# Kernel optimization log

Measured on AMD Instinct MI355X. Metric: run time of the kernel, lower is better.

## Reference

```python
import jax, jax.numpy as jnp
import numpy as np

NUM_RBF = 16
TOP_K = 30
MAXREL = 32  # max_relative_feature
M_CTX = 16   # ligand context atoms per residue

PT_GROUP = jnp.array([0,1,18,1,2,13,14,15,16,17,18,1,2,13,14,15,16,17,18,1,2,3,4,5,6,7,8,9,10,11,12,13,14,15,16,17,18,1,2,3,4,5,6,7,8,9,10,11,12,13,14,15,16,17,18,1,2,3,3,3,3,3,3,3,3,3,3,3,3,3,3,3,4,5,6,7,8,9,10,11,12,13,14,15,16,17,18,1,2,3,3,3,3,3,3,3,3,3,3,3,3,3,3,3,4,5,6,7,8,9,10,11,12,13,14,15,16,17,18], dtype=jnp.int32)
PT_PERIOD = jnp.array([0,1,1,2,2,2,2,2,2,2,2,3,3,3,3,3,3,3,3,4,4,4,4,4,4,4,4,4,4,4,4,4,4,4,4,4,4,5,5,5,5,5,5,5,5,5,5,5,5,5,5,5,5,5,5,6,6,6,6,6,6,6,6,6,6,6,6,6,6,6,6,6,6,6,6,6,6,6,6,6,6,6,6,6,6,6,6,7,7,7,7,7,7,7,7,7,7,7,7,7,7,7,7,7,7,7,7,7,7,7,7,7,7,7,7,7,7,7,7], dtype=jnp.int32)

# pair order after the Ca-Ca term: (N,N),(C,C),(O,O),(Cb,Cb),(Ca,N),(Ca,C),(Ca,O),(Ca,Cb),
# (N,C),(N,O),(N,Cb),(Cb,C),(Cb,O),(O,C),(N,Ca),(C,Ca),(O,Ca),(Cb,Ca),(C,N),(O,N),(Cb,N),(C,Cb),(O,Cb),(C,O)
# atom index in A5 stack: N=0, Ca=1, C=2, O=3, Cb=4
AI = np.array([0,2,3,4,1,1,1,1,0,0,0,4,4,3,0,2,3,4,2,3,4,2,3,2])
BI = np.array([0,2,3,4,0,2,3,4,2,3,4,2,3,2,1,1,1,1,0,0,0,4,4,3])


def _rbf(D):
    mu = jnp.linspace(2.0, 22.0, NUM_RBF)
    sigma = (22.0 - 2.0) / NUM_RBF
    return jnp.exp(-(((D[..., None] - mu) / sigma) ** 2))


def _angle_features(A, Bc, Cc, Y):
    v1 = A - Bc
    v2 = Cc - Bc
    e1 = v1 / jnp.linalg.norm(v1, axis=-1, keepdims=True)
    dot = jnp.einsum('bli,bli->bl', e1, v2)[..., None]
    u2 = v2 - e1 * dot
    e2 = u2 / jnp.linalg.norm(u2, axis=-1, keepdims=True)
    e3 = jnp.cross(e1, e2, axis=-1)
    R = jnp.concatenate((e1[..., None], e2[..., None], e3[..., None]), axis=-1)  # [B,L,3,3]
    lv = jnp.einsum('blqp,blyq->blyp', R, Y - Bc[:, :, None, :])
    rxy = jnp.sqrt(lv[..., 0] ** 2 + lv[..., 1] ** 2 + 1e-8)
    f1 = lv[..., 0] / rxy
    f2 = lv[..., 1] / rxy
    rxyz = jnp.linalg.norm(lv, axis=-1) + 1e-8
    f3 = rxy / rxyz
    f4 = lv[..., 2] / rxyz
    return jnp.stack([f1, f2, f3, f4], axis=-1)  # [B,L,M,4]


def setup_inputs() -> dict:
    key = jax.random.key(0)
    ks = jax.random.split(key, 16)
    B, L, M = 2, 2048, M_CTX
    X = jax.random.normal(ks[0], (B, L, 4, 3), jnp.float32) * 10.0
    Y = jax.random.normal(ks[1], (B, L, M, 3), jnp.float32) * 10.0
    mask = jnp.ones((B, L), jnp.float32)
    Y_m = jnp.ones((B, L, M), jnp.float32)
    R_idx = jnp.arange(B * L, dtype=jnp.int32).reshape(B, L)
    chain_labels = jax.random.randint(ks[2], (B, L), 0, 2, jnp.int32)
    Y_t = jax.random.randint(ks[3], (B, L, M), 1, 119, jnp.int32)
    def lin(k, fi, fo):
        return jax.random.normal(k, (fi, fo), jnp.float32) / np.sqrt(fi)
    params = dict(
        Wp=lin(ks[4], 2 * MAXREL + 2, 16), bp=jnp.zeros((16,), jnp.float32),
        We=lin(ks[5], 16 + 25 * NUM_RBF, 128), be=jnp.zeros((128,), jnp.float32),
        Wn=lin(ks[6], 5 * NUM_RBF + 64 + 4, 128), bn=jnp.zeros((128,), jnp.float32),
        Wt=lin(ks[7], 147, 64), bt=jnp.zeros((64,), jnp.float32),
        Wyn=lin(ks[8], 147, 128), byn=jnp.zeros((128,), jnp.float32),
        Wye=lin(ks[9], NUM_RBF, 128), bye=jnp.zeros((128,), jnp.float32),
    )
    return dict(X=X, Y=Y, mask=mask, Y_m=Y_m, R_idx=R_idx, chain_labels=chain_labels, Y_t=Y_t, **params)


def reference(X, Y, mask, Y_m, R_idx, chain_labels, Y_t,
              Wp, bp, We, be, Wn, bn, Wt, bt, Wyn, byn, Wye, bye):
    B, L = X.shape[0], X.shape[1]
    N, Ca, C, O = X[:, :, 0], X[:, :, 1], X[:, :, 2], X[:, :, 3]
    b_ = Ca - N
    c_ = C - Ca
    a_ = jnp.cross(b_, c_, axis=-1)
    Cb = -0.58273431 * a_ + 0.56802827 * b_ - 0.54067466 * c_ + Ca

    # masked pairwise distances + kNN (smallest-k)
    m2 = mask[:, None, :] * mask[:, :, None]
    dX = Ca[:, None, :, :] - Ca[:, :, None, :]
    D = m2 * jnp.sqrt(jnp.sum(dX * dX, -1) + 1e-6)
    Dadj = D + (1.0 - m2) * jnp.max(D, -1, keepdims=True)
    k = min(TOP_K, L)
    negD, E_idx = jax.lax.top_k(-Dadj, k)
    D_neighbors = -negD  # [B,L,K]

    # gather all 5 atom coords of neighbors once, then all 24 cross-atom RBFs
    A5 = jnp.stack([N, Ca, C, O, Cb], axis=2)  # [B,L,5,3]
    nb = A5[jnp.arange(B)[:, None, None], E_idx]  # [B,L,K,5,3]
    dvec = A5[:, :, None, AI, :] - nb[:, :, :, BI, :]  # [B,L,K,24,3]
    Dp = jnp.sqrt(jnp.sum(dvec * dvec, -1) + 1e-6)
    RBF_all = jnp.concatenate([_rbf(D_neighbors),
                               _rbf(Dp).reshape(B, L, k, 24 * NUM_RBF)], axis=-1)  # [B,L,K,400]

    # positional encodings
    offset = jnp.take_along_axis(R_idx[:, :, None] - R_idx[:, None, :], E_idx, axis=2)
    Ech = jnp.take_along_axis((chain_labels[:, :, None] == chain_labels[:, None, :]).astype(jnp.int32), E_idx, axis=2)
    d = jnp.clip(offset + MAXREL, 0, 2 * MAXREL)
    d = d * Ech + (1 - Ech) * (2 * MAXREL + 1)
    Epos = jax.nn.one_hot(d, 2 * MAXREL + 2, dtype=jnp.float32) @ Wp + bp
    E = jnp.concatenate([Epos, RBF_all], axis=-1) @ We + be  # [B,L,K,128]

    # ligand atom featurization
    g = PT_GROUP[Y_t]
    p = PT_PERIOD[Y_t]
    Yt1 = jnp.concatenate([jax.nn.one_hot(Y_t, 120, dtype=jnp.float32),
                           jax.nn.one_hot(g, 19, dtype=jnp.float32),
                           jax.nn.one_hot(p, 8, dtype=jnp.float32)], axis=-1)  # [B,L,M,147]
    Yt_lin = Yt1 @ Wt + bt  # [B,L,M,64]
    dAY = A5[:, :, :, None, :] - Y[:, :, None, :, :]  # [B,L,5,M,3]
    D_AY = jnp.sqrt(jnp.sum(dAY * dAY, -1) + 1e-6)
    RBF_AY = jnp.transpose(_rbf(D_AY), (0, 1, 3, 2, 4)).reshape(B, L, Y.shape[2], 5 * NUM_RBF)
    f_ang = _angle_features(N, Ca, C, Y)  # [B,L,M,4]
    V = jnp.concatenate([RBF_AY, Yt_lin, f_ang], axis=-1) @ Wn + bn  # [B,L,M,128]

    dYY = Y[:, :, :, None, :] - Y[:, :, None, :, :]
    Y_edges = _rbf(jnp.sqrt(jnp.sum(dYY * dYY, -1) + 1e-6)) @ Wye + bye  # [B,L,M,M,128]
    Y_nodes = Yt1 @ Wyn + byn  # [B,L,M,128]
    return V, E, E_idx, Y_nodes, Y_edges, Y_m
```

## Files before the change

kernel.cpp:

```cpp
#include <hip/hip_runtime.h>
#include <float.h>

typedef unsigned int   u32;
typedef unsigned short ushort_t;
typedef __attribute__((ext_vector_type(8))) short  bf16x8;
typedef __attribute__((ext_vector_type(4))) float  f32x4;
typedef __attribute__((ext_vector_type(8))) unsigned short ushort8;

#define NB 2
#define NL 2048
#define NM 16
#define NK 30

#define OV  0ull
#define OE  8388608ull
#define OEI 24117248ull
#define OYN 24240128ull
#define OYE 32628736ull
#define OYM 166846464ull

__constant__ int PT_GROUP_c[119] = {0,1,18,1,2,13,14,15,16,17,18,1,2,13,14,15,16,17,18,1,2,3,4,5,6,7,8,9,10,11,12,13,14,15,16,17,18,1,2,3,4,5,6,7,8,9,10,11,12,13,14,15,16,17,18,1,2,3,3,3,3,3,3,3,3,3,3,3,3,3,3,3,4,5,6,7,8,9,10,11,12,13,14,15,16,17,18,1,2,3,3,3,3,3,3,3,3,3,3,3,3,3,3,3,4,5,6,7,8,9,10,11,12,13,14,15,16,17,18};
__constant__ int PT_PERIOD_c[119] = {0,1,1,2,2,2,2,2,2,2,2,3,3,3,3,3,3,3,3,4,4,4,4,4,4,4,4,4,4,4,4,4,4,4,4,4,4,5,5,5,5,5,5,5,5,5,5,5,5,5,5,5,5,5,5,6,6,6,6,6,6,6,6,6,6,6,6,6,6,6,6,6,6,6,6,6,6,6,6,6,6,6,6,6,6,6,6,7,7,7,7,7,7,7,7,7,7,7,7,7,7,7,7,7,7,7,7,7,7,7,7,7,7,7,7,7,7,7,7};
__constant__ int AI_c[24] = {0,2,3,4,1,1,1,1,0,0,0,4,4,3,0,2,3,4,2,3,4,2,3,2};
__constant__ int BI_c[24] = {0,2,3,4,0,2,3,4,2,3,4,2,3,2,1,1,1,1,0,0,0,4,4,3};

__device__ __forceinline__ float cl24(float v) {
  return fminf(fmaxf(v, -24.f), 24.f);
}

__device__ __forceinline__ ushort_t f2bf(float f) {
  u32 u = __float_as_uint(f);
  return (ushort_t)((u + 0x7fffu + ((u >> 16) & 1u)) >> 16);
}

__device__ __forceinline__ float rbff(float d, int r) {
  float mu = 2.0f + (20.0f / 15.0f) * (float)r;
  float t = (d - mu) * 0.8f;
  return __expf(-t * t);
}

__global__ __launch_bounds__(256) void k_init(const float* __restrict__ We,
        const float* __restrict__ Wn, const float* __restrict__ X,
        ushort_t* __restrict__ WeT, ushort_t* __restrict__ WnT,
        float* __restrict__ A5, float* __restrict__ Ca4,
        float* __restrict__ Fr,
        const int* __restrict__ Y_t, const float* __restrict__ Wyn,
        const float* __restrict__ byn, const float* __restrict__ Y_m,
        float* __restrict__ out) {
  int blk = blockIdx.x;
  int tid = threadIdx.x;
  if (blk < 128) {
    int n = blk;
    int ntile = n >> 4, ln = n & 15;
    for (int k = tid; k < 416; k += 256) {
      int c = k >> 5, r = k & 31, hk = r >> 3, e = r & 7;
      WeT[(size_t)((ntile * 13 + c) * 512) + (hk * 16 + ln) * 8 + e] =
          f2bf(We[(size_t)k * 128 + n]);
    }
    return;
  }
  if (blk < 256) {
    int n = blk - 128;
    int ntile = n >> 4, ln = n & 15;
    if (tid < 160) {
      int c = tid >> 5, r = tid & 31, hk = r >> 3, e = r & 7;
      WnT[(size_t)((ntile * 5 + c) * 512) + (hk * 16 + ln) * 8 + e] =
          (tid < 148) ? f2bf(Wn[(size_t)tid * 128 + n]) : (ushort_t)0;
    }
    return;
  }
  if (blk < 272) {
    int id = (blk - 256) * 256 + tid;
    if (id >= NB * NL) return;
    const float* x = X + (size_t)id * 12;
    float Nx=x[0],Ny=x[1],Nz=x[2], Cax=x[3],Cay=x[4],Caz=x[5];
    float Cx=x[6],Cy=x[7],Cz=x[8], Ox=x[9],Oy=x[10],Oz=x[11];
    float bx=Cax-Nx, by=Cay-Ny, bz=Caz-Nz;
    float cx=Cx-Cax, cy=Cy-Cay, cz=Cz-Caz;
    float ax=by*cz-bz*cy, ay=bz*cx-bx*cz, az=bx*cy-by*cx;
    float Cbx = -0.58273431f*ax + 0.56802827f*bx - 0.54067466f*cx + Cax;
    float Cby = -0.58273431f*ay + 0.56802827f*by - 0.54067466f*cy + Cay;
    float Cbz = -0.58273431f*az + 0.56802827f*bz - 0.54067466f*cz + Caz;
    float* A = A5 + (size_t)id * 15;
    A[0]=Nx;A[1]=Ny;A[2]=Nz; A[3]=Cax;A[4]=Cay;A[5]=Caz;
    A[6]=Cx;A[7]=Cy;A[8]=Cz; A[9]=Ox;A[10]=Oy;A[11]=Oz;
    A[12]=Cbx;A[13]=Cby;A[14]=Cbz;
    Ca4[id*4+0]=Cax; Ca4[id*4+1]=Cay; Ca4[id*4+2]=Caz; Ca4[id*4+3]=0.f;
    float v1x=Nx-Cax, v1y=Ny-Cay, v1z=Nz-Caz;
    float v2x=Cx-Cax, v2y=Cy-Cay, v2z=Cz-Caz;
    float n1 = sqrtf(v1x*v1x+v1y*v1y+v1z*v1z);
    float e1x=v1x/n1, e1y=v1y/n1, e1z=v1z/n1;
    float dot = e1x*v2x+e1y*v2y+e1z*v2z;
    float u2x=v2x-e1x*dot, u2y=v2y-e1y*dot, u2z=v2z-e1z*dot;
    float n2 = sqrtf(u2x*u2x+u2y*u2y+u2z*u2z);
    float e2x=u2x/n2, e2y=u2y/n2, e2z=u2z/n2;
    float e3x=e1y*e2z-e1z*e2y, e3y=e1z*e2x-e1x*e2z, e3z=e1x*e2y-e1y*e2x;
    float* F = Fr + (size_t)id * 9;
    F[0]=e1x;F[1]=e1y;F[2]=e1z; F[3]=e2x;F[4]=e2y;F[5]=e2z; F[6]=e3x;F[7]=e3y;F[8]=e3z;
    return;
  }
  {
    int bl = blk - 272;
    if (tid < NM)
      out[OYM + (size_t)bl * NM + tid] = Y_m[(size_t)bl * NM + tid];
    int m = tid >> 4, n0 = (tid & 15) * 8;
    int yt = Y_t[(size_t)bl * NM + m];
    int g = PT_GROUP_c[yt], p = PT_PERIOD_c[yt];
    const float* w0 = Wyn + yt * 128 + n0;
    const float* w1 = Wyn + (120 + g) * 128 + n0;
    const float* w2 = Wyn + (139 + p) * 128 + n0;
    float4 r0 = *(const float4*)&w0[0], r1 = *(const float4*)&w0[4];
    float4 s0 = *(const float4*)&w1[0], s1 = *(const float4*)&w1[4];
    float4 t0 = *(const float4*)&w2[0], t1 = *(const float4*)&w2[4];
    float4 b0 = *(const float4*)&byn[n0], b1 = *(const float4*)&byn[n0 + 4];
    float4 o0, o1;
    o0.x = cl24(r0.x + s0.x + t0.x + b0.x);
    o0.y = cl24(r0.y + s0.y + t0.y + b0.y);
    o0.z = cl24(r0.z + s0.z + t0.z + b0.z);
    o0.w = cl24(r0.w + s0.w + t0.w + b0.w);
    o1.x = cl24(r1.x + s1.x + t1.x + b1.x);
    o1.y = cl24(r1.y + s1.y + t1.y + b1.y);
    o1.z = cl24(r1.z + s1.z + t1.z + b1.z);
    o1.w = cl24(r1.w + s1.w + t1.w + b1.w);
    size_t ob = OYN + ((size_t)bl * NM + m) * 128 + n0;
    *(float4*)&out[ob]     = o0;
    *(float4*)&out[ob + 4] = o1;
  }
}

__global__ __launch_bounds__(256) void k_topk(const float* __restrict__ Ca4,
                                              const float* __restrict__ mask,
                                              float* __restrict__ Dn,
                                              int* __restrict__ Eidx,
                                              float* __restrict__ out) {
  __shared__ float dist[NL];
  __shared__ float rv[4];
  __shared__ float cand_v[128];
  __shared__ int   cand_i[128];
  int row = blockIdx.x;
  int b = row >> 11;
  int tid = threadIdx.x;
  const float4* cab = (const float4*)Ca4 + ((size_t)b << 11);
  float4 ci = ((const float4*)Ca4)[row];
  float mi = mask[row];
  float lmax = 0.f;
  for (int j = tid; j < NL; j += 256) {
    float4 cj = cab[j];
    float dx = __fsub_rn(ci.x, cj.x);
    float dy = __fsub_rn(ci.y, cj.y);
    float dz = __fsub_rn(ci.z, cj.z);
    float s  = __fadd_rn(__fadd_rn(__fadd_rn(__fmul_rn(dx,dx), __fmul_rn(dy,dy)),
                                   __fmul_rn(dz,dz)), 1e-6f);
    float D  = __fmul_rn(__fmul_rn(mask[(b << 11) + j], mi), __fsqrt_rn(s));
    dist[j] = D;
    lmax = fmaxf(lmax, D);
  }
  #pragma unroll
  for (int s = 32; s > 0; s >>= 1) lmax = fmaxf(lmax, __shfl_xor(lmax, s));
  if ((tid & 63) == 0) rv[tid >> 6] = lmax;
  __syncthreads();
  float rowmax = fmaxf(fmaxf(rv[0], rv[1]), fmaxf(rv[2], rv[3]));
  for (int j = tid; j < NL; j += 256) {
    float mj = mask[(b << 11) + j];
    dist[j] = __fadd_rn(dist[j], __fmul_rn(__fsub_rn(1.f, __fmul_rn(mi, mj)), rowmax));
  }
  __syncthreads();
  int w = tid >> 6, l = tid & 63;
  int base = w * 512 + l;
  float v[8];
  #pragma unroll
  for (int k = 0; k < 8; k++) v[k] = dist[base + k * 64];
  if (tid < 8) { cand_v[120 + tid] = FLT_MAX; cand_i[120 + tid] = NL; }
  for (int it = 0; it < NK; it++) {
    float bv = FLT_MAX; int bj = NL;
    #pragma unroll
    for (int k = 0; k < 8; k++) {
      int jj = base + k * 64;
      if (v[k] < bv) { bv = v[k]; bj = jj; }
    }
    #pragma unroll
    for (int s = 32; s > 0; s >>= 1) {
      float ov = __shfl_xor(bv, s);
      int   oj = __shfl_xor(bj, s);
      if (ov < bv || (ov == bv && oj < bj)) { bv = ov; bj = oj; }
    }
    int ow = bj & 511;
    int ko = ow >> 6;
    bool mine = (ow & 63) == l;
    #pragma unroll
    for (int k = 0; k < 8; k++)
      if (mine && k == ko) v[k] = FLT_MAX;
    if (l == 0) { cand_v[w * NK + it] = bv; cand_i[w * NK + it] = bj; }
  }
  __syncthreads();
  if (tid < 64) {
    float v1 = cand_v[tid], v2 = cand_v[64 + tid];
    int   i1 = cand_i[tid], i2 = cand_i[64 + tid];
    for (int it = 0; it < NK; it++) {
      float bv; int bj, sl;
      if (v1 < v2 || (v1 == v2 && i1 < i2)) { bv = v1; bj = i1; sl = tid; }
      else                                  { bv = v2; bj = i2; sl = 64 + tid; }
      #pragma unroll
      for (int s = 32; s > 0; s >>= 1) {
        float ov = __shfl_xor(bv, s);
        int   oj = __shfl_xor(bj, s);
        int   os = __shfl_xor(sl, s);
        if (ov < bv || (ov == bv && oj < bj)) { bv = ov; bj = oj; sl = os; }
      }
      if (sl == tid)           v1 = FLT_MAX;
      else if (sl == 64 + tid) v2 = FLT_MAX;
      if (tid == 0) {
        Dn[(size_t)row * NK + it]   = bv;
        Eidx[(size_t)row * NK + it] = bj;
        out[OEI + (size_t)row * NK + it] = (float)bj;
      }
    }
  }
}

__global__ __launch_bounds__(256) void k_edge(const float* __restrict__ A5,
        const float* __restrict__ Dn, const int* __restrict__ Eidx,
        const int* __restrict__ R_idx, const int* __restrict__ cl,
        const float* __restrict__ Wp, const float* __restrict__ bp,
        const ushort_t* __restrict__ WeT, const float* __restrict__ be,
        float* __restrict__ out) {
  __shared__ __align__(16) ushort_t feat[32][424];
  int tid = threadIdx.x;
  int e0 = blockIdx.x * 32;
  {
    int el = tid >> 3;
    int te = tid & 7;
    int e  = e0 + el;
    int bi = e / NK;
    int b  = bi >> 11;
    int j  = Eidx[e];
    j = j < 0 ? 0 : (j > NL - 1 ? NL - 1 : j);
    int jrow = (b << 11) + j;
    const float* Ac = A5 + (size_t)bi * 15;
    const float* An = A5 + (size_t)jrow * 15;
    int off = R_idx[bi] - R_idx[jrow];
    int d;
    if (cl[bi] == cl[jrow]) { d = off + 32; d = d < 0 ? 0 : (d > 64 ? 64 : d); }
    else d = 65;
    feat[el][2*te]   = f2bf(Wp[d * 16 + 2*te]   + bp[2*te]);
    feat[el][2*te+1] = f2bf(Wp[d * 16 + 2*te+1] + bp[2*te+1]);
    float dn = Dn[e];
    feat[el][16 + 2*te]   = f2bf(rbff(dn, 2*te));
    feat[el][16 + 2*te+1] = f2bf(rbff(dn, 2*te+1));
    #pragma unroll
    for (int pp = 0; pp < 3; pp++) {
      int p = te + pp * 8;
      int ai = AI_c[p] * 3, bj2 = BI_c[p] * 3;
      float dx = Ac[ai]   - An[bj2];
      float dy = Ac[ai+1] - An[bj2+1];
      float dz = Ac[ai+2] - An[bj2+2];
      float dp = sqrtf(dx*dx + dy*dy + dz*dz + 1e-6f);
      int fb = 32 + p * 16;
      #pragma unroll
      for (int r = 0; r < 16; r++) feat[el][fb + r] = f2bf(rbff(dp, r));
    }
  }
  __syncthreads();
  int l  = tid & 63;
  int wid = tid >> 6;
  int wm = wid >> 1, wn = wid & 1;
  f32x4 acc0 = {0.f,0.f,0.f,0.f}, acc1 = {0.f,0.f,0.f,0.f};
  f32x4 acc2 = {0.f,0.f,0.f,0.f}, acc3 = {0.f,0.f,0.f,0.f};
  const ushort_t* Wb = WeT + l * 8;
  #pragma unroll 2
  for (int c = 0; c < 13; c++) {
    bf16x8 a  = *(const bf16x8*)&feat[wm*16 + (l & 15)][c*32 + (l >> 4)*8];
    bf16x8 b0 = *(const bf16x8*)(Wb + ((wn*4 + 0)*13 + c)*512);
    bf16x8 b1 = *(const bf16x8*)(Wb + ((wn*4 + 1)*13 + c)*512);
    bf16x8 b2 = *(const bf16x8*)(Wb + ((wn*4 + 2)*13 + c)*512);
    bf16x8 b3 = *(const bf16x8*)(Wb + ((wn*4 + 3)*13 + c)*512);
    acc0 = __builtin_amdgcn_mfma_f32_16x16x32_bf16(a, b0, acc0, 0, 0, 0);
    acc1 = __builtin_amdgcn_mfma_f32_16x16x32_bf16(a, b1, acc1, 0, 0, 0);
    acc2 = __builtin_amdgcn_mfma_f32_16x16x32_bf16(a, b2, acc2, 0, 0, 0);
    acc3 = __builtin_amdgcn_mfma_f32_16x16x32_bf16(a, b3, acc3, 0, 0, 0);
  }
  #pragma unroll
  for (int t = 0; t < 4; t++) {
    f32x4 av = (t==0) ? acc0 : (t==1) ? acc1 : (t==2) ? acc2 : acc3;
    int n = wn*64 + t*16 + (l & 15);
    float bb = be[n];
    #pragma unroll
    for (int jj = 0; jj < 4; jj++) {
      int ee = e0 + wm*16 + (l >> 4)*4 + jj;
      out[OE + (size_t)ee * 128 + n] = cl24(av[jj] + bb);
    }
  }
}

__global__ __launch_bounds__(256) void k_v(const float* __restrict__ A5,
        const float* __restrict__ Fr, const float* __restrict__ Y,
        const int* __restrict__ Y_t,
        const ushort_t* __restrict__ WnT, const float* __restrict__ bn,
        const float* __restrict__ Wt, const float* __restrict__ bt,
        float* __restrict__ out) {
  __shared__ __align__(16) ushort_t feat[16][168];
  __shared__ float dAY[16][8];
  int tid = threadIdx.x;
  int bl = blockIdx.x;
  if (tid < 80) {
    int m = tid / 5, a = tid % 5;
    float dx = A5[(size_t)bl*15 + a*3 + 0] - Y[(size_t)bl*48 + m*3 + 0];
    float dy = A5[(size_t)bl*15 + a*3 + 1] - Y[(size_t)bl*48 + m*3 + 1];
    float dz = A5[(size_t)bl*15 + a*3 + 2] - Y[(size_t)bl*48 + m*3 + 2];
    dAY[m][a] = sqrtf(dx*dx + dy*dy + dz*dz + 1e-6f);
  }
  __syncthreads();
  {
    int m = tid >> 4, q = tid & 15;
    #pragma unroll
    for (int a = 0; a < 5; a++) feat[m][a * 16 + q] = f2bf(rbff(dAY[m][a], q));
    int yt = Y_t[(size_t)bl * NM + m];
    int g = PT_GROUP_c[yt], p = PT_PERIOD_c[yt];
    {
      float4 wa = *(const float4*)&Wt[yt*64 + q*4];
      float4 wb = *(const float4*)&Wt[(120+g)*64 + q*4];
      float4 wc = *(const float4*)&Wt[(139+p)*64 + q*4];
      float4 bb = *(const float4*)&bt[q*4];
      feat[m][80 + q*4 + 0] = f2bf(wa.x + wb.x + wc.x + bb.x);
      feat[m][80 + q*4 + 1] = f2bf(wa.y + wb.y + wc.y + bb.y);
      feat[m][80 + q*4 + 2] = f2bf(wa.z + wb.z + wc.z + bb.z);
      feat[m][80 + q*4 + 3] = f2bf(wa.w + wb.w + wc.w + bb.w);
    }
    if (q == 0) {
      const float* fr = Fr + (size_t)bl * 9;
      float cax = A5[(size_t)bl*15+3], cay = A5[(size_t)bl*15+4], caz = A5[(size_t)bl*15+5];
      float yx = Y[(size_t)bl*48 + m*3+0] - cax;
      float yy = Y[(size_t)bl*48 + m*3+1] - cay;
      float yz = Y[(size_t)bl*48 + m*3+2] - caz;
      float l0 = fr[0]*yx + fr[1]*yy + fr[2]*yz;
      float l1 = fr[3]*yx + fr[4]*yy + fr[5]*yz;
      float l2 = fr[6]*yx + fr[7]*yy + fr[8]*yz;
      float rxy  = sqrtf(l0*l0 + l1*l1 + 1e-8f);
      float rxyz = sqrtf(l0*l0 + l1*l1 + l2*l2) + 1e-8f;
      feat[m][144] = f2bf(l0 / rxy);
      feat[m][145] = f2bf(l1 / rxy);
      feat[m][146] = f2bf(rxy / rxyz);
      feat[m][147] = f2bf(l2 / rxyz);
    }
    if (q < 12) feat[m][148 + q] = 0;
  }
  __syncthreads();
  int l = tid & 63;
  int wid = tid >> 6;
  int n0 = wid * 32;
  f32x4 acc0 = {0.f,0.f,0.f,0.f}, acc1 = {0.f,0.f,0.f,0.f};
  const ushort_t* Wb = WnT + l * 8;
  #pragma unroll
  for (int c = 0; c < 5; c++) {
    bf16x8 a  = *(const bf16x8*)&feat[l & 15][c*32 + (l >> 4)*8];
    bf16x8 b0 = *(const bf16x8*)(Wb + ((2*wid + 0)*5 + c)*512);
    bf16x8 b1 = *(const bf16x8*)(Wb + ((2*wid + 1)*5 + c)*512);
    acc0 = __builtin_amdgcn_mfma_f32_16x16x32_bf16(a, b0, acc0, 0, 0, 0);
    acc1 = __builtin_amdgcn_mfma_f32_16x16x32_bf16(a, b1, acc1, 0, 0, 0);
  }
  #pragma unroll
  for (int t = 0; t < 2; t++) {
    f32x4 av = (t==0) ? acc0 : acc1;
    int n = n0 + t*16 + (l & 15);
    float bb = bn[n];
    #pragma unroll
    for (int jj = 0; jj < 4; jj++) {
      int m = (l >> 4)*4 + jj;
      out[OV + ((size_t)bl * NM + m) * 128 + n] = cl24(av[jj] + bb);
    }
  }
}

__global__ __launch_bounds__(256) void k_yedge(const float* __restrict__ Y,
        const float* __restrict__ Wye, const float* __restrict__ bye,
        float* __restrict__ out) {
  __shared__ float rbf_s[128][20];
  __shared__ float wye_s[16][128];
  __shared__ float bye_s[128];
  int tid = threadIdx.x;
  int bl   = blockIdx.x >> 1;
  int half = blockIdx.x & 1;
  for (int x = tid; x < 2048; x += 256) wye_s[x >> 7][x & 127] = Wye[x];
  if (tid < 128) bye_s[tid] = bye[tid];
  {
    int lp = tid >> 1, rh = (tid & 1) * 8;
    int p = half * 128 + lp;
    int m = p >> 4, m2 = p & 15;
    const float* ya = Y + (size_t)bl * 48 + m * 3;
    const float* yb = Y + (size_t)bl * 48 + m2 * 3;
    float dx = ya[0]-yb[0], dy = ya[1]-yb[1], dz = ya[2]-yb[2];
    float dd = sqrtf(dx*dx + dy*dy + dz*dz + 1e-6f);
    #pragma unroll
    for (int r = 0; r < 8; r++) rbf_s[lp][rh + r] = rbff(dd, rh + r);
  }
  __syncthreads();
  int n2 = (tid & 63) * 2;
  int pg = tid >> 6;
  float wy0[16], wy1[16];
  #pragma unroll
  for (int k = 0; k < 16; k++) { wy0[k] = wye_s[k][n2]; wy1[k] = wye_s[k][n2+1]; }
  float bb0 = bye_s[n2], bb1 = bye_s[n2+1];
  size_t obase = OYE + (size_t)bl * (NM * NM * 128) + (size_t)half * 128 * 128;
  for (int lp = pg * 32; lp < pg * 32 + 32; lp++) {
    float s0 = bb0, s1 = bb1;
    #pragma unroll
    for (int k4 = 0; k4 < 4; k4++) {
      float4 rv = *(const float4*)&rbf_s[lp][k4 * 4];
      s0 = fmaf(rv.x, wy0[k4*4+0], s0); s1 = fmaf(rv.x, wy1[k4*4+0], s1);
      s0 = fmaf(rv.y, wy0[k4*4+1], s0); s1 = fmaf(rv.y, wy1[k4*4+1], s1);
      s0 = fmaf(rv.z, wy0[k4*4+2], s0); s1 = fmaf(rv.z, wy1[k4*4+2], s1);
      s0 = fmaf(rv.w, wy0[k4*4+3], s0); s1 = fmaf(rv.w, wy1[k4*4+3], s1);
    }
    float2 st; st.x = cl24(s0); st.y = cl24(s1);
    *(float2*)&out[obase + (size_t)lp * 128 + n2] = st;
  }
}

extern "C" void kernel_launch(void* const* d_in, const int* in_sizes, int n_in,
                              void* d_out, int out_size, void* d_ws, size_t ws_size,
                              hipStream_t stream) {
  const float* X     = (const float*)d_in[0];
  const float* Y     = (const float*)d_in[1];
  const float* mask  = (const float*)d_in[2];
  const float* Y_m   = (const float*)d_in[3];
  const int*   R_idx = (const int*)d_in[4];
  const int*   cl    = (const int*)d_in[5];
  const int*   Y_t   = (const int*)d_in[6];
  const float* Wp    = (const float*)d_in[7];
  const float* bp    = (const float*)d_in[8];
  const float* We    = (const float*)d_in[9];
  const float* be    = (const float*)d_in[10];
  const float* Wn    = (const float*)d_in[11];
  const float* bn    = (const float*)d_in[12];
  const float* Wt    = (const float*)d_in[13];
  const float* bt    = (const float*)d_in[14];
  const float* Wyn   = (const float*)d_in[15];
  const float* byn   = (const float*)d_in[16];
  const float* Wye   = (const float*)d_in[17];
  const float* bye   = (const float*)d_in[18];
  float* out = (float*)d_out;

  float* wsf  = (float*)d_ws;
  float* A5   = wsf;
  float* Ca4  = A5  + 61440;
  float* Fr   = Ca4 + 16384;
  float* Dn   = Fr  + 36864;
  int*   Eidx = (int*)(Dn + 122880);
  ushort_t* WeT = (ushort_t*)(Eidx + 122880);
  ushort_t* WnT = WeT + 128 * 416;

  k_init <<<272 + NB*NL, 256, 0, stream>>>(We, Wn, X, WeT, WnT, A5, Ca4, Fr,
                                           Y_t, Wyn, byn, Y_m, out);
  k_topk <<<NB*NL, 256, 0, stream>>>(Ca4, mask, Dn, Eidx, out);
  k_edge <<<(NB*NL*NK)/32, 256, 0, stream>>>(A5, Dn, Eidx, R_idx, cl,
                                             Wp, bp, WeT, be, out);
  k_v    <<<NB*NL, 256, 0, stream>>>(A5, Fr, Y, Y_t, WnT, bn, Wt, bt, out);
  k_yedge<<<2*NB*NL, 256, 0, stream>>>(Y, Wye, bye, out);
}
```

Baseline: 291.2 us.

## Fuse top-k neighbor selection with edge feature GEMM kernel

Merges the top-k neighbor search and edge featurization/MFMA projection into one kernel per residue row. Neighbor distances and indices stay in shared memory instead of round-tripping through global workspace, and one kernel launch is removed. Shared memory is aliased between the distance array and the feature tile. In exchange, each block handles only 30 edges in a 32-row tile, wasting some MFMA work, and the larger shared footprint may lower occupancy.

```diff
diff --git a/kernel.cpp b/kernel.cpp
--- a/kernel.cpp
+++ b/kernel.cpp
@@ -128,18 +128,25 @@
   }
 }
 
-__global__ __launch_bounds__(256) void k_topk(const float* __restrict__ Ca4,
-                                              const float* __restrict__ mask,
-                                              float* __restrict__ Dn,
-                                              int* __restrict__ Eidx,
-                                              float* __restrict__ out) {
-  __shared__ float dist[NL];
-  __shared__ float rv[4];
-  __shared__ float cand_v[128];
-  __shared__ int   cand_i[128];
+__global__ __launch_bounds__(256) void k_topk_edge(
+        const float* __restrict__ Ca4, const float* __restrict__ mask,
+        const float* __restrict__ A5,
+        const int* __restrict__ R_idx, const int* __restrict__ cl,
+        const float* __restrict__ Wp, const float* __restrict__ bp,
+        const ushort_t* __restrict__ WeT, const float* __restrict__ be,
+        float* __restrict__ out) {
+  extern __shared__ __align__(16) char smem[];
+  float* dist              = (float*)smem;
+  ushort_t (*feat)[424]    = (ushort_t(*)[424])smem;
+  float* rv                = (float*)(smem + 27136);
+  float* cand_v            = (float*)(smem + 27152);
+  int*   cand_i            = (int*)(smem + 27664);
+  float* ed_d              = (float*)(smem + 28176);
+  int*   ed_i              = (int*)(smem + 28296);
   int row = blockIdx.x;
   int b = row >> 11;
   int tid = threadIdx.x;
+
   const float4* cab = (const float4*)Ca4 + ((size_t)b << 11);
   float4 ci = ((const float4*)Ca4)[row];
   float mi = mask[row];
@@ -210,58 +217,46 @@
       if (sl == tid)           v1 = FLT_MAX;
       else if (sl == 64 + tid) v2 = FLT_MAX;
       if (tid == 0) {
-        Dn[(size_t)row * NK + it]   = bv;
-        Eidx[(size_t)row * NK + it] = bj;
+        ed_d[it] = bv;
+        ed_i[it] = bj;
         out[OEI + (size_t)row * NK + it] = (float)bj;
       }
     }
   }
-}
-
-__global__ __launch_bounds__(256) void k_edge(const float* __restrict__ A5,
-        const float* __restrict__ Dn, const int* __restrict__ Eidx,
-        const int* __restrict__ R_idx, const int* __restrict__ cl,
-        const float* __restrict__ Wp, const float* __restrict__ bp,
-        const ushort_t* __restrict__ WeT, const float* __restrict__ be,
-        float* __restrict__ out) {
-  __shared__ __align__(16) ushort_t feat[32][424];
-  int tid = threadIdx.x;
-  int e0 = blockIdx.x * 32;
+  __syncthreads();
   {
     int el = tid >> 3;
     int te = tid & 7;
-    int e  = e0 + el;
-    int bi = e / NK;
-    int b  = bi >> 11;
-    int j  = Eidx[e];
-    j = j < 0 ? 0 : (j > NL - 1 ? NL - 1 : j);
-    int jrow = (b << 11) + j;
-    const float* Ac = A5 + (size_t)bi * 15;
-    const float* An = A5 + (size_t)jrow * 15;
-    int off = R_idx[bi] - R_idx[jrow];
-    int d;
-    if (cl[bi] == cl[jrow]) { d = off + 32; d = d < 0 ? 0 : (d > 64 ? 64 : d); }
-    else d = 65;
-    feat[el][2*te]   = f2bf(Wp[d * 16 + 2*te]   + bp[2*te]);
-    feat[el][2*te+1] = f2bf(Wp[d * 16 + 2*te+1] + bp[2*te+1]);
-    float dn = Dn[e];
-    feat[el][16 + 2*te]   = f2bf(rbff(dn, 2*te));
-    feat[el][16 + 2*te+1] = f2bf(rbff(dn, 2*te+1));
-    #pragma unroll
-    for (int pp = 0; pp < 3; pp++) {
-      int p = te + pp * 8;
-      int ai = AI_c[p] * 3, bj2 = BI_c[p] * 3;
-      float dx = Ac[ai]   - An[bj2];
-      float dy = Ac[ai+1] - An[bj2+1];
-      float dz = Ac[ai+2] - An[bj2+2];
-      float dp = sqrtf(dx*dx + dy*dy + dz*dz + 1e-6f);
-      int fb = 32 + p * 16;
+    if (el < NK) {
+      int j = ed_i[el];
+      j = j < 0 ? 0 : (j > NL - 1 ? NL - 1 : j);
+      int jrow = (b << 11) + j;
+      const float* Ac = A5 + (size_t)row * 15;
+      const float* An = A5 + (size_t)jrow * 15;
+      int off = R_idx[row] - R_idx[jrow];
+      int d;
+      if (cl[row] == cl[jrow]) { d = off + 32; d = d < 0 ? 0 : (d > 64 ? 64 : d); }
+      else d = 65;
+      feat[el][2*te]   = f2bf(Wp[d * 16 + 2*te]   + bp[2*te]);
+      feat[el][2*te+1] = f2bf(Wp[d * 16 + 2*te+1] + bp[2*te+1]);
+      float dn = ed_d[el];
+      feat[el][16 + 2*te]   = f2bf(rbff(dn, 2*te));
+      feat[el][16 + 2*te+1] = f2bf(rbff(dn, 2*te+1));
       #pragma unroll
-      for (int r = 0; r < 16; r++) feat[el][fb + r] = f2bf(rbff(dp, r));
-    }
-  }
-  __syncthreads();
-  int l  = tid & 63;
+      for (int pp = 0; pp < 3; pp++) {
+        int p = te + pp * 8;
+        int ai = AI_c[p] * 3, bj2 = BI_c[p] * 3;
+        float dx = Ac[ai]   - An[bj2];
+        float dy = Ac[ai+1] - An[bj2+1];
+        float dz = Ac[ai+2] - An[bj2+2];
+        float dp = sqrtf(dx*dx + dy*dy + dz*dz + 1e-6f);
+        int fb = 32 + p * 16;
+        #pragma unroll
+        for (int r = 0; r < 16; r++) feat[el][fb + r] = f2bf(rbff(dp, r));
+      }
+    }
+  }
+  __syncthreads();
   int wid = tid >> 6;
   int wm = wid >> 1, wn = wid & 1;
   f32x4 acc0 = {0.f,0.f,0.f,0.f}, acc1 = {0.f,0.f,0.f,0.f};
@@ -286,8 +281,9 @@
     float bb = be[n];
     #pragma unroll
     for (int jj = 0; jj < 4; jj++) {
-      int ee = e0 + wm*16 + (l >> 4)*4 + jj;
-      out[OE + (size_t)ee * 128 + n] = cl24(av[jj] + bb);
+      int ee = wm*16 + (l >> 4)*4 + jj;
+      if (ee < NK)
+        out[OE + ((size_t)row * NK + ee) * 128 + n] = cl24(av[jj] + bb);
     }
   }
 }
@@ -444,15 +440,12 @@
   float* A5   = wsf;
   float* Ca4  = A5  + 61440;
   float* Fr   = Ca4 + 16384;
-  float* Dn   = Fr  + 36864;
-  int*   Eidx = (int*)(Dn + 122880);
-  ushort_t* WeT = (ushort_t*)(Eidx + 122880);
+  ushort_t* WeT = (ushort_t*)(Fr + 36864);
   ushort_t* WnT = WeT + 128 * 416;
 
   k_init <<<272 + NB*NL, 256, 0, stream>>>(We, Wn, X, WeT, WnT, A5, Ca4, Fr,
                                            Y_t, Wyn, byn, Y_m, out);
-  k_topk <<<NB*NL, 256, 0, stream>>>(Ca4, mask, Dn, Eidx, out);
-  k_edge <<<(NB*NL*NK)/32, 256, 0, stream>>>(A5, Dn, Eidx, R_idx, cl,
+  k_topk_edge<<<NB*NL, 256, 28416, stream>>>(Ca4, mask, A5, R_idx, cl,
                                              Wp, bp, WeT, be, out);
   k_v    <<<NB*NL, 256, 0, stream>>>(A5, Fr, Y, Y_t, WnT, bn, Wt, bt, out);
   k_yedge<<<2*NB*NL, 256, 0, stream>>>(Y, Wye, bye, out);
```

Result: slower. 341.2 us (+17.2%).
